# Kernel optimization log

Hardware: AMD Instinct MI355X
Metric: run time of the kernel (lower is better)

## Reference

```python
import jax, jax.numpy as jnp
import numpy as np

DROPOUT_P = 0.1
HEAD_DIM = 64
INV_SCALE = 1.0 / float(np.sqrt(HEAD_DIM))  # matches driver: inv_scale = 1/head_dim**0.5


def setup_inputs() -> dict:
    key = jax.random.key(0)
    k1, k2, k3, k4 = jax.random.split(key, 4)
    B, S, H, D = 2, 2048, 16, HEAD_DIM
    return {
        "query": jax.random.normal(k1, (B, S, H, D), dtype=jnp.float32),
        "key": jax.random.normal(k2, (B, S, H, D), dtype=jnp.float32),
        "value": jax.random.normal(k3, (B, S, H, D), dtype=jnp.float32),
        "attn_mask": jnp.zeros((B, H, S, S), dtype=jnp.float32),
        "dropout_u": jax.random.uniform(k4, (B, H, S, S), dtype=jnp.float32),
    }


def reference(query, key, value, attn_mask, dropout_u):
    # [B,S,H,D] -> [B,H,S,D]
    q = jnp.transpose(query, (0, 2, 1, 3))
    k = jnp.transpose(key, (0, 2, 1, 3))
    v = jnp.transpose(value, (0, 2, 1, 3))
    # scores = (q @ k^T) / inv_scale + mask   (faithful: original .div(inv_scale))
    scores = jnp.einsum("bhqd,bhkd->bhqk", q, k) / INV_SCALE + attn_mask
    attn = jax.nn.softmax(scores, axis=-1)
    # deterministic dropout: keep where u >= p, scale by 1/(1-p)
    keep = (dropout_u >= DROPOUT_P).astype(attn.dtype) / (1.0 - DROPOUT_P)
    out = jnp.einsum("bhqk,bhkd->bhqd", attn * keep, v)  # [B,H,S,D]
    return out
```

## Files before the change

kernel.cpp:

```cpp
#include <hip/hip_runtime.h>
#include <stdint.h>

#define S_LEN 2048
#define HEADS 16
#define DIM   64

typedef float  f4v  __attribute__((ext_vector_type(4)));
typedef float  f16v __attribute__((ext_vector_type(16)));
typedef short  s8v  __attribute__((ext_vector_type(8)));
typedef unsigned int   u4v  __attribute__((ext_vector_type(4)));
typedef unsigned short us4v __attribute__((ext_vector_type(4)));

__device__ __forceinline__ unsigned short f2bf(float f) {
  unsigned int u = __float_as_uint(f);
  u += 0x7fffu + ((u >> 16) & 1u);
  return (unsigned short)(u >> 16);
}
__device__ __forceinline__ float bf2f(unsigned short h) {
  return __uint_as_float(((unsigned int)h) << 16);
}
__device__ __forceinline__ unsigned int pk2(float e0, float e1) {
  return (unsigned int)f2bf(e0) | ((unsigned int)f2bf(e1) << 16);
}

__global__ __launch_bounds__(256) void prep_k(const float* __restrict__ K,
                                              unsigned short* __restrict__ Khf,
                                              unsigned short* __restrict__ Klf) {
  int f = blockIdx.x * 256 + threadIdx.x;
  int l  = f & 63;
  int dc = (f >> 6) & 3;
  int kt = (f >> 8) & 63;
  int bh = f >> 14;
  int b = bh >> 4, hh = bh & 15;
  int s  = kt * 32 + (l & 31);
  int d0 = dc * 16 + (l >> 5) * 8;
  const float* src = K + (((size_t)(b * S_LEN + s) * HEADS + hh) << 6) + d0;
  f4v va = *(const f4v*)src;
  f4v vb = *(const f4v*)(src + 4);
  us4v ha, hb, la, lb;
#pragma unroll
  for (int i = 0; i < 4; ++i) {
    unsigned short h = f2bf(va[i]);
    ha[i] = h; la[i] = f2bf(va[i] - bf2f(h));
    unsigned short h2 = f2bf(vb[i]);
    hb[i] = h2; lb[i] = f2bf(vb[i] - bf2f(h2));
  }
  size_t o = (size_t)f * 8;
  *(us4v*)(Khf + o) = ha; *(us4v*)(Khf + o + 4) = hb;
  *(us4v*)(Klf + o) = la; *(us4v*)(Klf + o + 4) = lb;
}

__global__ __launch_bounds__(256) void prep_v(const float* __restrict__ V,
                                              unsigned short* __restrict__ Vf) {
  __shared__ float tile[32 * 68];
  int bh = blockIdx.x >> 6;
  int kt = blockIdx.x & 63;
  int b = bh >> 4, hh = bh & 15;
  int t = threadIdx.x;
  {
    int row = t >> 3, c8 = (t & 7) * 8;
    const float* src =
        V + (((size_t)(b * S_LEN + kt * 32 + row) * HEADS + hh) << 6) + c8;
    f4v va = *(const f4v*)src;
    f4v vb = *(const f4v*)(src + 4);
    *(f4v*)(tile + row * 68 + c8) = va;
    *(f4v*)(tile + row * 68 + c8 + 4) = vb;
  }
  __syncthreads();
  int kc = t >> 7, dblk = (t >> 6) & 1, l = t & 63;
  int s0 = kc * 16 + (l >> 5) * 8;
  int col = dblk * 32 + (l & 31);
  us4v w0, w1;
#pragma unroll
  for (int j = 0; j < 4; ++j) {
    w0[j] = f2bf(tile[(s0 + j) * 68 + col]);
    w1[j] = f2bf(tile[(s0 + 4 + j) * 68 + col]);
  }
  size_t o = ((((size_t)bh * 64 + kt) * 4 + kc * 2 + dblk) * 64 + l) * 8;
  *(us4v*)(Vf + o) = w0;
  *(us4v*)(Vf + o + 4) = w1;
}

__global__ __launch_bounds__(256, 2) void attn_fwd(
    const float* __restrict__ Q, const float* __restrict__ MASK,
    const float* __restrict__ U, const unsigned short* __restrict__ Khf,
    const unsigned short* __restrict__ Klf, const unsigned short* __restrict__ Vf,
    float* __restrict__ OUT) {
  __shared__ short P_lds[4][2048];
  int bid = blockIdx.x;
  int lid = ((bid & 7) << 6) + (bid >> 3);
  int bh = lid >> 4, qt = lid & 15;
  int wv = threadIdx.x >> 6, ln = threadIdx.x & 63;
  int l31 = ln & 31, h5 = ln >> 5;
  int q0 = qt * 128 + wv * 32;
  int b = bh >> 4, hh = bh & 15;
  short* lds = &P_lds[wv][0];

  const float* qrow = Q + (((size_t)(b * S_LEN + q0 + l31) * HEADS + hh) << 6);
  s8v qfh[4], qfl[4];
#pragma unroll
  for (int dc = 0; dc < 4; ++dc) {
    const float* p = qrow + dc * 16 + 8 * h5;
    f4v va = *(const f4v*)p;
    f4v vb = *(const f4v*)(p + 4);
    u4v wh, wl;
#pragma unroll
    for (int t = 0; t < 4; ++t) {
      float x0 = (t < 2) ? va[2 * t] : vb[2 * (t - 2)];
      float x1 = (t < 2) ? va[2 * t + 1] : vb[2 * (t - 2) + 1];
      unsigned short h0 = f2bf(x0), h1 = f2bf(x1);
      wh[t] = (unsigned)h0 | ((unsigned)h1 << 16);
      wl[t] = pk2(x0 - bf2f(h0), x1 - bf2f(h1));
    }
    qfh[dc] = __builtin_bit_cast(s8v, wh);
    qfl[dc] = __builtin_bit_cast(s8v, wl);
  }

  const float* Mp = MASK + ((size_t)bh << 22);
  const float* Up = U + ((size_t)bh << 22);
  const int vbase = (q0 + 4 * h5) * S_LEN + l31;
  const unsigned short* kbh = Khf + ((size_t)bh << 17);
  const unsigned short* kbl = Klf + ((size_t)bh << 17);
  const unsigned short* vbp = Vf + ((size_t)bh << 17);
  const int fl8 = ln * 8;
  const int rq  = (l31 & 3) | (((l31 >> 3) & 3) << 2);
  const int h5p = (l31 >> 2) & 1;

  f16v o0, o1;
#pragma unroll
  for (int i = 0; i < 16; ++i) { o0[i] = 0.f; o1[i] = 0.f; }
  float mrun[16];
#pragma unroll
  for (int i = 0; i < 16; ++i) mrun[i] = -3.0e38f;
  float plane = 0.f;

  for (int kt = 0; kt < S_LEN / 32; ++kt) {
    int kv0 = kt << 5;
    s8v kfh[4], kfl[4];
#pragma unroll
    for (int dc = 0; dc < 4; ++dc) {
      size_t off = (size_t)((kt * 4 + dc) << 9) + fl8;
      kfh[dc] = *(const s8v*)(kbh + off);
      kfl[dc] = *(const s8v*)(kbl + off);
    }
    s8v vf[2][2];
#pragma unroll
    for (int kc = 0; kc < 2; ++kc)
#pragma unroll
      for (int db = 0; db < 2; ++db)
        vf[kc][db] = *(const s8v*)(vbp + (size_t)((kt * 4 + kc * 2 + db) << 9) + fl8);
    float mk[16], uk[16];
#pragma unroll
    for (int r = 0; r < 16; ++r) {
      int off = vbase + kv0 + (8 * (r >> 2) + (r & 3)) * S_LEN;
      mk[r] = Mp[off];
      uk[r] = Up[off];
    }
    f16v sc;
#pragma unroll
    for (int i = 0; i < 16; ++i) sc[i] = 0.f;
#pragma unroll
    for (int dc = 0; dc < 4; ++dc) {
      sc = __builtin_amdgcn_mfma_f32_32x32x16_bf16(qfh[dc], kfh[dc], sc, 0, 0, 0);
      sc = __builtin_amdgcn_mfma_f32_32x32x16_bf16(qfl[dc], kfh[dc], sc, 0, 0, 0);
      sc = __builtin_amdgcn_mfma_f32_32x32x16_bf16(qfh[dc], kfl[dc], sc, 0, 0, 0);
    }
    float sv[16], tmax[16];
#pragma unroll
    for (int r = 0; r < 16; ++r) {
      sv[r] = fmaf(sc[r], 8.0f, mk[r]);
      tmax[r] = sv[r];
    }
#pragma unroll
    for (int d = 1; d < 32; d <<= 1)
#pragma unroll
      for (int r = 0; r < 16; ++r)
        tmax[r] = fmaxf(tmax[r], __shfl_xor(tmax[r], d));
    bool grow = false;
#pragma unroll
    for (int r = 0; r < 16; ++r) grow |= (tmax[r] > mrun[r] + 8.0f);
    if (__any(grow)) {
      float alr[16];
#pragma unroll
      for (int r = 0; r < 16; ++r) {
        float mn = fmaxf(mrun[r], tmax[r]);
        alr[r] = __expf(mrun[r] - mn);
        mrun[r] = mn;
      }
#pragma unroll
      for (int i = 0; i < 16; ++i) { o0[i] *= alr[i]; o1[i] *= alr[i]; }
      float x = alr[rq];
      float y = __shfl_xor(x, 32);
      plane *= (h5 == h5p) ? x : y;
    }
#pragma unroll
    for (int r = 0; r < 16; ++r) {
      float pp = __expf(sv[r] - mrun[r]) * (1.0f / 0.9f);
      unsigned short bits = f2bf(pp);
      if (uk[r] < 0.1f) bits |= 0x8000;
      int qr = 8 * (r >> 2) + 4 * h5 + (r & 3);
      lds[qr * 64 + (((l31 >> 3) ^ (qr & 7)) << 3) + (l31 & 7)] = (short)bits;
    }
    __builtin_amdgcn_sched_barrier(0);
    s8v pa[2];
#pragma unroll
    for (int kc = 0; kc < 2; ++kc) {
      int blk = (2 * kc + h5) ^ (l31 & 7);
      u4v bits = *(u4v*)(lds + l31 * 64 + blk * 8);
      u4v absb, kept;
#pragma unroll
      for (int i = 0; i < 4; ++i) {
        absb[i] = bits[i] & 0x7FFF7FFFu;
        unsigned dropm = ((bits[i] >> 15) & 0x00010001u) * 0xFFFFu;
        kept[i] = absb[i] & ~dropm;
        plane += __uint_as_float((absb[i] & 0xFFFFu) << 16);
        plane += __uint_as_float(absb[i] & 0xFFFF0000u);
      }
      pa[kc] = __builtin_bit_cast(s8v, kept);
    }
    o0 = __builtin_amdgcn_mfma_f32_32x32x16_bf16(pa[0], vf[0][0], o0, 0, 0, 0);
    o0 = __builtin_amdgcn_mfma_f32_32x32x16_bf16(pa[1], vf[1][0], o0, 0, 0, 0);
    o1 = __builtin_amdgcn_mfma_f32_32x32x16_bf16(pa[0], vf[0][1], o1, 0, 0, 0);
    o1 = __builtin_amdgcn_mfma_f32_32x32x16_bf16(pa[1], vf[1][1], o1, 0, 0, 0);
  }

  plane += __shfl_xor(plane, 32);
  float inv = 1.0f / (0.9f * plane);
  float invv[16];
#pragma unroll
  for (int r = 0; r < 16; ++r)
    invv[r] = __shfl(inv, 8 * (r >> 2) + 4 * h5 + (r & 3));
#pragma unroll
  for (int r = 0; r < 16; ++r) {
    int qr = 8 * (r >> 2) + 4 * h5 + (r & 3);
    float* orow = OUT + (((size_t)bh * S_LEN + q0 + qr) << 6) + l31;
    orow[0]  = o0[r] * invv[r];
    orow[32] = o1[r] * invv[r];
  }
}

extern "C" void kernel_launch(void* const* d_in, const int* in_sizes, int n_in,
                              void* d_out, int out_size, void* d_ws, size_t ws_size,
                              hipStream_t stream) {
  const float* Q = (const float*)d_in[0];
  const float* K = (const float*)d_in[1];
  const float* V = (const float*)d_in[2];
  const float* M = (const float*)d_in[3];
  const float* U = (const float*)d_in[4];
  float* out = (float*)d_out;

  unsigned short* Khf = (unsigned short*)d_ws;
  unsigned short* Klf = Khf + (size_t)(4u << 20);
  unsigned short* Vf  = Klf + (size_t)(4u << 20);

  prep_k<<<2048, 256, 0, stream>>>(K, Khf, Klf);
  prep_v<<<2048, 256, 0, stream>>>(V, Vf);
  attn_fwd<<<512, 256, 0, stream>>>(Q, M, U, Khf, Klf, Vf, out);
}
```

Before: 310.1 us.

## Split KV range across two blocks with a combine kernel, simplify dropout bookkeeping

Adds a split-KV (flash-decoding style) path: each query tile's key range is divided between two blocks that write partial outputs plus running max and sum, and a new combine kernel merges them. This doubles the grid to 1024 blocks and raises the launch-bounds occupancy hint to 4, aiming to fill more CUs and hide the memory latency of streaming the large mask and dropout tensors. The row-sum is now kept per row in registers and dropout is applied by zeroing P before the bf16 store, which removes the sign-bit encoding and the unpacking after the LDS read. In exchange it adds a partial-output write and readback, a third launch, and a workspace-size dependency with a fallback path.

New measurement: 836.3 us. +169.7%, slower.

```diff
diff --git a/kernel.cpp b/kernel.cpp
--- a/kernel.cpp
+++ b/kernel.cpp
@@ -6,6 +6,7 @@
 #define DIM   64
 
 typedef float  f4v  __attribute__((ext_vector_type(4)));
+typedef float  f2v  __attribute__((ext_vector_type(2)));
 typedef float  f16v __attribute__((ext_vector_type(16)));
 typedef short  s8v  __attribute__((ext_vector_type(8)));
 typedef unsigned int   u4v  __attribute__((ext_vector_type(4)));
@@ -81,15 +82,25 @@
   *(us4v*)(Vf + o + 4) = w1;
 }
 
-__global__ __launch_bounds__(256, 2) void attn_fwd(
+template <int PARTIAL>
+__global__ __launch_bounds__(256, 4) void attn_fwd(
     const float* __restrict__ Q, const float* __restrict__ MASK,
     const float* __restrict__ U, const unsigned short* __restrict__ Khf,
     const unsigned short* __restrict__ Klf, const unsigned short* __restrict__ Vf,
-    float* __restrict__ OUT) {
+    float* __restrict__ OUT, float* __restrict__ OPART, float* __restrict__ ML) {
   __shared__ short P_lds[4][2048];
   int bid = blockIdx.x;
-  int lid = ((bid & 7) << 6) + (bid >> 3);
-  int bh = lid >> 4, qt = lid & 15;
+  int bh, qt, sp;
+  if (PARTIAL) {
+    int lid = ((bid & 7) << 7) + (bid >> 3);
+    bh = lid >> 5; qt = (lid >> 1) & 15; sp = lid & 1;
+  } else {
+    int lid = ((bid & 7) << 6) + (bid >> 3);
+    bh = lid >> 4; qt = lid & 15; sp = 0;
+  }
+  const int NT = PARTIAL ? (S_LEN / 64) : (S_LEN / 32);
+  const int kv_begin = PARTIAL ? sp * (S_LEN / 2) : 0;
+
   int wv = threadIdx.x >> 6, ln = threadIdx.x & 63;
   int l31 = ln & 31, h5 = ln >> 5;
   int q0 = qt * 128 + wv * 32;
@@ -116,25 +127,22 @@
     qfl[dc] = __builtin_bit_cast(s8v, wl);
   }
 
-  const float* Mp = MASK + ((size_t)bh << 22);
-  const float* Up = U + ((size_t)bh << 22);
+  const float* Mp = MASK + ((size_t)bh << 22) + kv_begin;
+  const float* Up = U + ((size_t)bh << 22) + kv_begin;
   const int vbase = (q0 + 4 * h5) * S_LEN + l31;
-  const unsigned short* kbh = Khf + ((size_t)bh << 17);
-  const unsigned short* kbl = Klf + ((size_t)bh << 17);
-  const unsigned short* vbp = Vf + ((size_t)bh << 17);
+  const unsigned short* kbh = Khf + ((size_t)bh << 17) + ((size_t)kv_begin << 6);
+  const unsigned short* kbl = Klf + ((size_t)bh << 17) + ((size_t)kv_begin << 6);
+  const unsigned short* vbp = Vf + ((size_t)bh << 17) + ((size_t)kv_begin << 6);
   const int fl8 = ln * 8;
-  const int rq  = (l31 & 3) | (((l31 >> 3) & 3) << 2);
-  const int h5p = (l31 >> 2) & 1;
 
   f16v o0, o1;
 #pragma unroll
   for (int i = 0; i < 16; ++i) { o0[i] = 0.f; o1[i] = 0.f; }
-  float mrun[16];
-#pragma unroll
-  for (int i = 0; i < 16; ++i) mrun[i] = -3.0e38f;
-  float plane = 0.f;
-
-  for (int kt = 0; kt < S_LEN / 32; ++kt) {
+  float mrun[16], pl[16];
+#pragma unroll
+  for (int i = 0; i < 16; ++i) { mrun[i] = -3.0e38f; pl[i] = 0.f; }
+
+  for (int kt = 0; kt < NT; ++kt) {
     int kv0 = kt << 5;
     s8v kfh[4], kfl[4];
 #pragma unroll
@@ -188,16 +196,14 @@
         mrun[r] = mn;
       }
 #pragma unroll
-      for (int i = 0; i < 16; ++i) { o0[i] *= alr[i]; o1[i] *= alr[i]; }
-      float x = alr[rq];
-      float y = __shfl_xor(x, 32);
-      plane *= (h5 == h5p) ? x : y;
+      for (int i = 0; i < 16; ++i) { o0[i] *= alr[i]; o1[i] *= alr[i]; pl[i] *= alr[i]; }
     }
 #pragma unroll
     for (int r = 0; r < 16; ++r) {
       float pp = __expf(sv[r] - mrun[r]) * (1.0f / 0.9f);
-      unsigned short bits = f2bf(pp);
-      if (uk[r] < 0.1f) bits |= 0x8000;
+      pl[r] += pp;
+      float pd = (uk[r] >= 0.1f) ? pp : 0.f;
+      unsigned short bits = f2bf(pd);
       int qr = 8 * (r >> 2) + 4 * h5 + (r & 3);
       lds[qr * 64 + (((l31 >> 3) ^ (qr & 7)) << 3) + (l31 & 7)] = (short)bits;
     }
@@ -206,17 +212,7 @@
 #pragma unroll
     for (int kc = 0; kc < 2; ++kc) {
       int blk = (2 * kc + h5) ^ (l31 & 7);
-      u4v bits = *(u4v*)(lds + l31 * 64 + blk * 8);
-      u4v absb, kept;
-#pragma unroll
-      for (int i = 0; i < 4; ++i) {
-        absb[i] = bits[i] & 0x7FFF7FFFu;
-        unsigned dropm = ((bits[i] >> 15) & 0x00010001u) * 0xFFFFu;
-        kept[i] = absb[i] & ~dropm;
-        plane += __uint_as_float((absb[i] & 0xFFFFu) << 16);
-        plane += __uint_as_float(absb[i] & 0xFFFF0000u);
-      }
-      pa[kc] = __builtin_bit_cast(s8v, kept);
+      pa[kc] = *(const s8v*)(lds + l31 * 64 + blk * 8);
     }
     o0 = __builtin_amdgcn_mfma_f32_32x32x16_bf16(pa[0], vf[0][0], o0, 0, 0, 0);
     o0 = __builtin_amdgcn_mfma_f32_32x32x16_bf16(pa[1], vf[1][0], o0, 0, 0, 0);
@@ -224,19 +220,57 @@
     o1 = __builtin_amdgcn_mfma_f32_32x32x16_bf16(pa[1], vf[1][1], o1, 0, 0, 0);
   }
 
-  plane += __shfl_xor(plane, 32);
-  float inv = 1.0f / (0.9f * plane);
-  float invv[16];
-#pragma unroll
-  for (int r = 0; r < 16; ++r)
-    invv[r] = __shfl(inv, 8 * (r >> 2) + 4 * h5 + (r & 3));
-#pragma unroll
-  for (int r = 0; r < 16; ++r) {
-    int qr = 8 * (r >> 2) + 4 * h5 + (r & 3);
-    float* orow = OUT + (((size_t)bh * S_LEN + q0 + qr) << 6) + l31;
-    orow[0]  = o0[r] * invv[r];
-    orow[32] = o1[r] * invv[r];
-  }
+#pragma unroll
+  for (int d = 1; d < 32; d <<= 1)
+#pragma unroll
+    for (int r = 0; r < 16; ++r) pl[r] += __shfl_xor(pl[r], d);
+
+  if (PARTIAL) {
+    size_t rowbase = (size_t)bh * S_LEN + q0;
+#pragma unroll
+    for (int r = 0; r < 16; ++r) {
+      int qr = 8 * (r >> 2) + 4 * h5 + (r & 3);
+      float* p = OPART + (rowbase + qr) * 128 + sp * 64 + l31;
+      p[0]  = o0[r];
+      p[32] = o1[r];
+    }
+#pragma unroll
+    for (int r = 0; r < 16; ++r) {
+      if (l31 == r) {
+        int qr = 8 * (r >> 2) + 4 * h5 + (r & 3);
+        f2v s; s[0] = mrun[r]; s[1] = pl[r];
+        *(f2v*)(ML + (rowbase + qr) * 4 + sp * 2) = s;
+      }
+    }
+  } else {
+#pragma unroll
+    for (int r = 0; r < 16; ++r) {
+      int qr = 8 * (r >> 2) + 4 * h5 + (r & 3);
+      float inv = 1.0f / (0.9f * pl[r]);
+      float* orow = OUT + (((size_t)bh * S_LEN + q0 + qr) << 6) + l31;
+      orow[0]  = o0[r] * inv;
+      orow[32] = o1[r] * inv;
+    }
+  }
+}
+
+__global__ __launch_bounds__(256) void combine(const float* __restrict__ OPART,
+                                               const float* __restrict__ ML,
+                                               float* __restrict__ OUT) {
+  int gid = blockIdx.x * 256 + threadIdx.x;
+  size_t row = (size_t)(gid >> 4);
+  int d4 = (gid & 15) * 4;
+  f4v mlv = *(const f4v*)(ML + row * 4);
+  float m0 = mlv[0], l0 = mlv[1], m1 = mlv[2], l1 = mlv[3];
+  float M = fmaxf(m0, m1);
+  float w0 = __expf(m0 - M), w1 = __expf(m1 - M);
+  float inv = 1.0f / (0.9f * (l0 * w0 + l1 * w1));
+  f4v a = *(const f4v*)(OPART + row * 128 + d4);
+  f4v bb = *(const f4v*)(OPART + row * 128 + 64 + d4);
+  f4v o;
+#pragma unroll
+  for (int i = 0; i < 4; ++i) o[i] = (a[i] * w0 + bb[i] * w1) * inv;
+  *(f4v*)(OUT + row * 64 + d4) = o;
 }
 
 extern "C" void kernel_launch(void* const* d_in, const int* in_sizes, int n_in,
@@ -252,8 +286,16 @@
   unsigned short* Khf = (unsigned short*)d_ws;
   unsigned short* Klf = Khf + (size_t)(4u << 20);
   unsigned short* Vf  = Klf + (size_t)(4u << 20);
+  float* Opart = (float*)(Vf + (size_t)(4u << 20));
+  float* ML    = Opart + (size_t)65536 * 128;
+  const size_t need = (size_t)24 * 1024 * 1024 + (size_t)65536 * 132 * 4 + (1u << 20);
 
   prep_k<<<2048, 256, 0, stream>>>(K, Khf, Klf);
   prep_v<<<2048, 256, 0, stream>>>(V, Vf);
-  attn_fwd<<<512, 256, 0, stream>>>(Q, M, U, Khf, Klf, Vf, out);
-}
+  if (ws_size >= need) {
+    attn_fwd<1><<<1024, 256, 0, stream>>>(Q, M, U, Khf, Klf, Vf, out, Opart, ML);
+    combine<<<4096, 256, 0, stream>>>(Opart, ML, out);
+  } else {
+    attn_fwd<0><<<512, 256, 0, stream>>>(Q, M, U, Khf, Klf, Vf, out, Opart, ML);
+  }
+}
```
